# Kernel tuning notes

Hardware: AMD Instinct MI355X
Metric: run time of the kernel (lower is better)

The kernel has to match this reference:

```python
import jax, jax.numpy as jnp
from jax import lax
import numpy as np
import math

EMBED_DIM = 1024
NUM_HEADS = 16
REDUCTION = 2


def setup_inputs() -> dict:
    key = jax.random.key(0)
    ks = jax.random.split(key, 11)
    B, N, C = 2, 4096, EMBED_DIM
    s = 1.0 / math.sqrt(C)
    return {
        "x": jax.random.normal(ks[0], (B, N, C), jnp.float32),
        "q_w": jax.random.normal(ks[1], (C, C), jnp.float32) * s,
        "q_b": jax.random.normal(ks[2], (C,), jnp.float32) * s,
        "k_w": jax.random.normal(ks[3], (C, C), jnp.float32) * s,
        "k_b": jax.random.normal(ks[4], (C,), jnp.float32) * s,
        "v_w": jax.random.normal(ks[5], (C, C), jnp.float32) * s,
        "v_b": jax.random.normal(ks[6], (C,), jnp.float32) * s,
        "conv_w": jax.random.normal(ks[7], (C, 1, 3), jnp.float32) * 0.5,
        "conv_b": jax.random.normal(ks[8], (C,), jnp.float32) * 0.1,
        "out_w": jax.random.normal(ks[9], (C, C), jnp.float32) * s,
        "out_b": jax.random.normal(ks[10], (C,), jnp.float32) * s,
    }


def reference(x, q_w, q_b, k_w, k_b, v_w, v_b, conv_w, conv_b, out_w, out_b):
    B, N, C = x.shape
    H = NUM_HEADS
    D = C // H
    scale = 1.0 / math.sqrt(D)

    q = x @ q_w.T + q_b  # [B,N,C]

    # depthwise conv1d KV downsample: kernel=3, stride=REDUCTION, pad=1, groups=C
    xd = jnp.transpose(x, (0, 2, 1))  # [B,C,N]
    xd = lax.conv_general_dilated(
        xd, conv_w, window_strides=(REDUCTION,), padding=[(1, 1)],
        feature_group_count=C, dimension_numbers=("NCH", "OIH", "NCH"))
    xd = xd + conv_b[None, :, None]
    xd = jnp.transpose(xd, (0, 2, 1))  # [B,Nk,C]

    k = xd @ k_w.T + k_b
    v = xd @ v_w.T + v_b

    Nk = k.shape[1]
    q = q.reshape(B, N, H, D).transpose(0, 2, 1, 3)   # [B,H,N,D]
    k = k.reshape(B, Nk, H, D).transpose(0, 2, 1, 3)  # [B,H,Nk,D]
    v = v.reshape(B, Nk, H, D).transpose(0, 2, 1, 3)

    att = jnp.einsum("bhnd,bhmd->bhnm", q, k) * scale  # [B,H,N,Nk]
    att = jax.nn.softmax(att, axis=-1)
    out = jnp.einsum("bhnm,bhmd->bhnd", att, v)        # [B,H,N,D]
    out = out.transpose(0, 2, 1, 3).reshape(B, N, C)
    return out @ out_w.T + out_b
```

## Files before the change

### kernel.cpp

```cpp
#include <hip/hip_runtime.h>
#include <stdint.h>
#include <stddef.h>


using bf16x8 = __attribute__((ext_vector_type(8))) short;
using f32x4  = __attribute__((ext_vector_type(4))) float;
using f32x16 = __attribute__((ext_vector_type(16))) float;
using u16x4  = __attribute__((ext_vector_type(4))) unsigned short;
using u32x4  = __attribute__((ext_vector_type(4))) uint32_t;

#if defined(__has_builtin)
#if __has_builtin(__builtin_amdgcn_exp2f)
#define FAST_EXP2(x) __builtin_amdgcn_exp2f(x)
#endif
#endif
#ifndef FAST_EXP2
extern "C" __device__ float __ocml_native_exp2_f32(float);
#define FAST_EXP2(x) __ocml_native_exp2_f32(x)
#endif

__device__ __forceinline__ unsigned short f2bf(float f) {
  union { float f; uint32_t u; } v; v.f = f;
  uint32_t r = v.u + 0x7fffu + ((v.u >> 16) & 1u);
  return (unsigned short)(r >> 16);
}

__device__ __forceinline__ uint32_t cvt_pk_bf16(float lo, float hi) {
  uint32_t r;
  asm("v_cvt_pk_bf16_f32 %0, %1, %2" : "=v"(r) : "v"(lo), "v"(hi));
  return r;
}

__device__ __forceinline__ void plane32_swap(uint32_t& a, uint32_t& b) {
  asm("v_permlane32_swap_b32 %0, %1" : "+v"(a), "+v"(b));
}

__global__ __launch_bounds__(256)
void cast_bf16_kernel(const float* __restrict__ in, unsigned short* __restrict__ out, int n) {
  int i = (blockIdx.x * 256 + threadIdx.x) * 8;
  if (i >= n) return;
  float4 a = *(const float4*)(in + i);
  float4 b = *(const float4*)(in + i + 4);
  u16x4 r0 = {f2bf(a.x), f2bf(a.y), f2bf(a.z), f2bf(a.w)};
  u16x4 r1 = {f2bf(b.x), f2bf(b.y), f2bf(b.z), f2bf(b.w)};
  *(u16x4*)(out + i) = r0;
  *(u16x4*)(out + i + 4) = r1;
}

struct WPtrs { const float* p0; const float* p1; const float* p2; const float* p3; };
__global__ __launch_bounds__(256)
void cast4_bf16_kernel(WPtrs in, unsigned short* __restrict__ out) {
  int which = blockIdx.x >> 9;
  int i = ((blockIdx.x & 511) * 256 + threadIdx.x) * 8;
  const float* src = (which == 0) ? in.p0 : (which == 1) ? in.p1
                   : (which == 2) ? in.p2 : in.p3;
  unsigned short* dst = out + (size_t)which * 1048576;
  float4 a = *(const float4*)(src + i);
  float4 b = *(const float4*)(src + i + 4);
  u16x4 r0 = {f2bf(a.x), f2bf(a.y), f2bf(a.z), f2bf(a.w)};
  u16x4 r1 = {f2bf(b.x), f2bf(b.y), f2bf(b.z), f2bf(b.w)};
  *(u16x4*)(dst + i) = r0;
  *(u16x4*)(dst + i + 4) = r1;
}

__global__ __launch_bounds__(256)
void conv_ds_kernel(const float* __restrict__ x, const float* __restrict__ cw,
                    const float* __restrict__ cb, unsigned short* __restrict__ xd) {
  int row = blockIdx.x;
  int b = row >> 11, m = row & 2047;
  int c = threadIdx.x * 4;
  const float* xb = x + (size_t)b * 4096 * 1024;
  int n0 = 2 * m - 1;
  float4 x0 = {0.f, 0.f, 0.f, 0.f};
  if (n0 >= 0) x0 = *(const float4*)(xb + (size_t)n0 * 1024 + c);
  float4 x1 = *(const float4*)(xb + (size_t)(2 * m) * 1024 + c);
  float4 x2 = *(const float4*)(xb + (size_t)(2 * m + 1) * 1024 + c);
  float4 w0 = *(const float4*)(cw + c * 3);
  float4 w1 = *(const float4*)(cw + c * 3 + 4);
  float4 w2 = *(const float4*)(cw + c * 3 + 8);
  float4 bb = *(const float4*)(cb + c);
  float r0 = x0.x * w0.x + x1.x * w0.y + x2.x * w0.z + bb.x;
  float r1 = x0.y * w0.w + x1.y * w1.x + x2.y * w1.y + bb.y;
  float r2 = x0.z * w1.z + x1.z * w1.w + x2.z * w2.x + bb.z;
  float r3 = x0.w * w2.y + x1.w * w2.z + x2.w * w2.w + bb.w;
  u16x4 r = {f2bf(r0), f2bf(r1), f2bf(r2), f2bf(r3)};
  *(u16x4*)(xd + (size_t)row * 1024 + c) = r;
}

template<int OUT_MODE>
__global__ __launch_bounds__(256)
void gemm_bt(const unsigned short* __restrict__ A, const unsigned short* __restrict__ W,
             const float* __restrict__ bias, const float* __restrict__ bias2,
             void* __restrict__ out, void* __restrict__ out2,
             int M, int N, int K) {
  __shared__ unsigned short As[128 * 32];
  __shared__ unsigned short Bs[128 * 32];
  const int tid = threadIdx.x;
  const int w = tid >> 6, lane = tid & 63;
  const int nbn = N >> 7;
  const int bm = blockIdx.x / nbn, bn = blockIdx.x % nbn;
  const int wr = w >> 1, wc = w & 1;
  const int l15 = lane & 15, l4 = lane >> 4;

  f32x4 acc[4][4];
#pragma unroll
  for (int m = 0; m < 4; ++m)
#pragma unroll
    for (int n = 0; n < 4; ++n) acc[m][n] = (f32x4)0.0f;

  const int arow = bm * 128 + w * 16 + (lane >> 2);
  const int brow = bn * 128 + w * 16 + (lane >> 2);
  const int kcol = (lane & 3) * 8;

  for (int kt = 0; kt < K; kt += 32) {
#pragma unroll
    for (int p = 0; p < 2; ++p) {
      __builtin_amdgcn_global_load_lds(
          (const __attribute__((address_space(1))) void*)(A + (size_t)(arow + p * 64) * K + kt + kcol),
          (__attribute__((address_space(3))) void*)(As + p * 2048 + w * 512), 16, 0, 0);
      __builtin_amdgcn_global_load_lds(
          (const __attribute__((address_space(1))) void*)(W + (size_t)(brow + p * 64) * K + kt + kcol),
          (__attribute__((address_space(3))) void*)(Bs + p * 2048 + w * 512), 16, 0, 0);
    }
    __syncthreads();
    bf16x8 af[4], bf[4];
#pragma unroll
    for (int m = 0; m < 4; ++m) af[m] = *(const bf16x8*)(As + (wr * 64 + m * 16 + l15) * 32 + l4 * 8);
#pragma unroll
    for (int n = 0; n < 4; ++n) bf[n] = *(const bf16x8*)(Bs + (wc * 64 + n * 16 + l15) * 32 + l4 * 8);
#pragma unroll
    for (int m = 0; m < 4; ++m)
#pragma unroll
      for (int n = 0; n < 4; ++n)
        acc[m][n] = __builtin_amdgcn_mfma_f32_16x16x32_bf16(af[m], bf[n], acc[m][n], 0, 0, 0);
    __syncthreads();
  }

  const bool vregion = (OUT_MODE == 3) && (bn >= 8);
#pragma unroll
  for (int n = 0; n < 4; ++n) {
    int col = bn * 128 + wc * 64 + n * 16 + l15;
    float bv = vregion ? bias2[col - 1024] : bias[col];
#pragma unroll
    for (int m = 0; m < 4; ++m) {
      int row0 = bm * 128 + wr * 64 + m * 16 + l4 * 4;
      if (vregion) {
        int b = row0 >> 11, kv = row0 & 2047;
        u16x4 r = {f2bf(acc[m][n][0] + bv), f2bf(acc[m][n][1] + bv),
                   f2bf(acc[m][n][2] + bv), f2bf(acc[m][n][3] + bv)};
        *(u16x4*)((unsigned short*)out2 + ((size_t)(b * 1024 + (col - 1024))) * 2048 + kv) = r;
      } else if (OUT_MODE == 1 || OUT_MODE == 3) {
        const int ldn = (OUT_MODE == 3) ? 1024 : N;
#pragma unroll
        for (int i = 0; i < 4; ++i)
          ((unsigned short*)out)[(size_t)(row0 + i) * ldn + col] = f2bf(acc[m][n][i] + bv);
      } else {
#pragma unroll
        for (int i = 0; i < 4; ++i)
          ((float*)out)[(size_t)(row0 + i) * N + col] = acc[m][n][i] + bv;
      }
    }
  }
}

#define ATT_SCL_L2E 0.18033688011112043f

__global__ __launch_bounds__(256)
void flash_attn_kernel(const unsigned short* __restrict__ q,
                       const unsigned short* __restrict__ k,
                       const unsigned short* __restrict__ vt,
                       unsigned short* __restrict__ o) {
  const int bid = blockIdx.x;
  const int lin = (bid & 7) * 128 + (bid >> 3);
  const int qb = lin & 31;
  const int hb = lin >> 5;
  const int h = hb & 15, b = hb >> 4;

  const int tid = threadIdx.x;
  const int w = tid >> 6, lane = tid & 63;
  const int l31 = lane & 31, hi = lane >> 5;

  __shared__ unsigned short Ks[2][64 * 64];
  __shared__ unsigned short Vs[2][64 * 64];

  const size_t C = 1024;
  const int qrow = b * 4096 + qb * 128 + w * 32 + l31;

  bf16x8 qf[4];
#pragma unroll
  for (int ks = 0; ks < 4; ++ks)
    qf[ks] = *(const bf16x8*)(q + (size_t)qrow * C + h * 64 + ks * 16 + hi * 8);

  f32x16 o0 = (f32x16)0.0f, o1 = (f32x16)0.0f;
  float lrun = 0.f;

  const int srow = (tid & 7) | ((tid >> 5) << 3);
  const int sc2  = (tid >> 3) & 3;
  const int sxor = (srow & 7);
  const unsigned short* kbase = k  + ((size_t)(b * 2048 + srow)) * C + h * 64;
  const unsigned short* vbase = vt + ((size_t)(b * 1024 + h * 64 + srow)) * 2048;

  bf16x8 krg[2], vrg[2], tmp[2];
#pragma unroll
  for (int j = 0; j < 2; ++j) tmp[j] = *(const bf16x8*)(kbase + (sc2 + 4 * j) * 8);
#pragma unroll
  for (int j = 0; j < 2; ++j)
    *(bf16x8*)(&Ks[0][srow * 64 + (((sc2 + 4 * j) ^ sxor) * 8)]) = tmp[j];
#pragma unroll
  for (int j = 0; j < 2; ++j) tmp[j] = *(const bf16x8*)(kbase + (size_t)64 * C + (sc2 + 4 * j) * 8);
#pragma unroll
  for (int j = 0; j < 2; ++j)
    *(bf16x8*)(&Ks[1][srow * 64 + (((sc2 + 4 * j) ^ sxor) * 8)]) = tmp[j];
#pragma unroll
  for (int j = 0; j < 2; ++j) tmp[j] = *(const bf16x8*)(vbase + (sc2 + 4 * j) * 8);
#pragma unroll
  for (int j = 0; j < 2; ++j)
    *(bf16x8*)(&Vs[0][srow * 64 + (((sc2 + 4 * j) ^ sxor) * 8)]) = tmp[j];
#pragma unroll
  for (int j = 0; j < 2; ++j) {
    krg[j] = *(const bf16x8*)(kbase + (size_t)128 * C + (sc2 + 4 * j) * 8);
    vrg[j] = *(const bf16x8*)(vbase + 64 + (sc2 + 4 * j) * 8);
  }
  __syncthreads();

  const int r0 = l31, r1 = 32 + l31;
  const int x0c = (r0 & 7) * 8, x1c = (r1 & 7) * 8;

  f32x16 sA0 = (f32x16)0.0f, sA1 = (f32x16)0.0f;
  f32x16 sB0 = (f32x16)0.0f, sB1 = (f32x16)0.0f;
  __builtin_amdgcn_s_setprio(1);
#pragma unroll
  for (int ks = 0; ks < 4; ++ks) {
    int coff = ks * 16 + hi * 8;
    bf16x8 kf0 = *(const bf16x8*)(&Ks[0][r0 * 64 + (coff ^ x0c)]);
    bf16x8 kf1 = *(const bf16x8*)(&Ks[0][r1 * 64 + (coff ^ x1c)]);
    sA0 = __builtin_amdgcn_mfma_f32_32x32x16_bf16(kf0, qf[0 + ks - ks], sA0, 0, 0, 0);
    sA0 = sA0;
    sA0 = __builtin_amdgcn_mfma_f32_32x32x16_bf16(kf0, qf[ks], sA0, 0, 0, 0);
    sA1 = __builtin_amdgcn_mfma_f32_32x32x16_bf16(kf1, qf[ks], sA1, 0, 0, 0);
  }
  __builtin_amdgcn_s_setprio(0);
  sA0 = (f32x16)0.0f; sA1 = (f32x16)0.0f;
  __builtin_amdgcn_s_setprio(1);
#pragma unroll
  for (int ks = 0; ks < 4; ++ks) {
    int coff = ks * 16 + hi * 8;
    bf16x8 kf0 = *(const bf16x8*)(&Ks[0][r0 * 64 + (coff ^ x0c)]);
    bf16x8 kf1 = *(const bf16x8*)(&Ks[0][r1 * 64 + (coff ^ x1c)]);
    sA0 = __builtin_amdgcn_mfma_f32_32x32x16_bf16(kf0, qf[ks], sA0, 0, 0, 0);
    sA1 = __builtin_amdgcn_mfma_f32_32x32x16_bf16(kf1, qf[ks], sA1, 0, 0, 0);
  }
  __builtin_amdgcn_s_setprio(0);
  __syncthreads();

  auto body = [&](int t, f32x16& c0, f32x16& c1, f32x16& n0, f32x16& n1) {
    const unsigned short* Vc = Vs[t & 1];

    if (t < 31) {
      const unsigned short* Kn = Ks[(t + 1) & 1];
      n0 = (f32x16)0.0f; n1 = (f32x16)0.0f;
      __builtin_amdgcn_s_setprio(1);
#pragma unroll
      for (int ks = 0; ks < 4; ++ks) {
        int coff = ks * 16 + hi * 8;
        bf16x8 kf0 = *(const bf16x8*)(Kn + r0 * 64 + (coff ^ x0c));
        bf16x8 kf1 = *(const bf16x8*)(Kn + r1 * 64 + (coff ^ x1c));
        n0 = __builtin_amdgcn_mfma_f32_32x32x16_bf16(kf0, qf[ks], n0, 0, 0, 0);
        n1 = __builtin_amdgcn_mfma_f32_32x32x16_bf16(kf1, qf[ks], n1, 0, 0, 0);
      }
      __builtin_amdgcn_s_setprio(0);
    }

    float rs0 = 0.f, rs1 = 0.f;
#pragma unroll
    for (int i = 0; i < 16; ++i) {
      float p0 = FAST_EXP2(c0[i] * ATT_SCL_L2E);
      float p1 = FAST_EXP2(c1[i] * ATT_SCL_L2E);
      c0[i] = p0; c1[i] = p1;
      rs0 += p0; rs1 += p1;
    }
    lrun += rs0 + rs1;

    u32x4 pw[4];
#pragma unroll
    for (int hh = 0; hh < 2; ++hh) {
#pragma unroll
      for (int cp = 0; cp < 2; ++cp) {
#pragma unroll
        for (int e = 0; e < 2; ++e) {
          float xa0 = (hh == 0) ? c0[8 * cp + 2 * e]     : c1[8 * cp + 2 * e];
          float xa1 = (hh == 0) ? c0[8 * cp + 2 * e + 1] : c1[8 * cp + 2 * e + 1];
          float xb0 = (hh == 0) ? c0[8 * cp + 4 + 2 * e]     : c1[8 * cp + 4 + 2 * e];
          float xb1 = (hh == 0) ? c0[8 * cp + 4 + 2 * e + 1] : c1[8 * cp + 4 + 2 * e + 1];
          uint32_t wa = cvt_pk_bf16(xa0, xa1);
          uint32_t wb = cvt_pk_bf16(xb0, xb1);
          plane32_swap(wa, wb);
          pw[2 * hh + cp][e]     = wa;
          pw[2 * hh + cp][e + 2] = wb;
        }
      }
    }

    __builtin_amdgcn_s_setprio(1);
#pragma unroll
    for (int ksv = 0; ksv < 4; ++ksv) {
      bf16x8 pv = __builtin_bit_cast(bf16x8, pw[ksv]);
      int coff = ksv * 16 + hi * 8;
      bf16x8 vf0 = *(const bf16x8*)(Vc + r0 * 64 + (coff ^ x0c));
      bf16x8 vf1 = *(const bf16x8*)(Vc + r1 * 64 + (coff ^ x1c));
      o0 = __builtin_amdgcn_mfma_f32_32x32x16_bf16(vf0, pv, o0, 0, 0, 0);
      o1 = __builtin_amdgcn_mfma_f32_32x32x16_bf16(vf1, pv, o1, 0, 0, 0);
    }
    __builtin_amdgcn_s_setprio(0);

    if (t < 30) {
#pragma unroll
      for (int j = 0; j < 2; ++j)
        *(bf16x8*)(&((unsigned short*)Ks[t & 1])[srow * 64 + (((sc2 + 4 * j) ^ sxor) * 8)]) = krg[j];
    }
    if (t < 31) {
#pragma unroll
      for (int j = 0; j < 2; ++j)
        *(bf16x8*)(&((unsigned short*)Vs[(t + 1) & 1])[srow * 64 + (((sc2 + 4 * j) ^ sxor) * 8)]) = vrg[j];
    }
    if (t < 29) {
#pragma unroll
      for (int j = 0; j < 2; ++j)
        krg[j] = *(const bf16x8*)(kbase + (size_t)(t + 3) * 64 * C + (sc2 + 4 * j) * 8);
    }
    if (t < 30) {
#pragma unroll
      for (int j = 0; j < 2; ++j)
        vrg[j] = *(const bf16x8*)(vbase + (t + 2) * 64 + (sc2 + 4 * j) * 8);
    }
    if (t < 31) __syncthreads();
  };

  for (int tt = 0; tt < 16; ++tt) {
    body(2 * tt,     sA0, sA1, sB0, sB1);
    body(2 * tt + 1, sB0, sB1, sA0, sA1);
  }

  float lsum = lrun + __shfl_xor(lrun, 32);
  const float inv = 1.0f / lsum;
  u32x4 ow[4];
#pragma unroll
  for (int c = 0; c < 4; ++c) {
#pragma unroll
    for (int e = 0; e < 2; ++e) {
      uint32_t wa = cvt_pk_bf16(o0[4 * c + 2 * e] * inv, o0[4 * c + 2 * e + 1] * inv);
      uint32_t wb = cvt_pk_bf16(o1[4 * c + 2 * e] * inv, o1[4 * c + 2 * e + 1] * inv);
      plane32_swap(wa, wb);
      ow[c][e]     = wa;
      ow[c][e + 2] = wb;
    }
  }
  unsigned short* op = o + (size_t)qrow * C + h * 64 + hi * 32;
#pragma unroll
  for (int ch = 0; ch < 4; ++ch)
    *(u32x4*)(op + ch * 8) = ow[ch];
}

extern "C" void kernel_launch(void* const* d_in, const int* in_sizes, int n_in,
                              void* d_out, int out_size, void* d_ws, size_t ws_size,
                              hipStream_t stream) {
  const float* x   = (const float*)d_in[0];
  const float* q_w = (const float*)d_in[1];
  const float* q_b = (const float*)d_in[2];
  const float* k_w = (const float*)d_in[3];
  const float* k_b = (const float*)d_in[4];
  const float* v_w = (const float*)d_in[5];
  const float* v_b = (const float*)d_in[6];
  const float* cw  = (const float*)d_in[7];
  const float* cb  = (const float*)d_in[8];
  const float* o_w = (const float*)d_in[9];
  const float* o_b = (const float*)d_in[10];
  float* out = (float*)d_out;

  unsigned short* ws    = (unsigned short*)d_ws;
  unsigned short* x_bf  = ws;
  unsigned short* qw_bf = x_bf + 8388608;
  unsigned short* kw_bf = qw_bf + 1048576;
  unsigned short* vw_bf = kw_bf + 1048576;
  unsigned short* ow_bf = vw_bf + 1048576;
  unsigned short* q_bf  = ow_bf + 1048576;
  unsigned short* xd_bf = q_bf + 8388608;
  unsigned short* k_bf  = xd_bf + 4194304;
  unsigned short* vt_bf = k_bf + 4194304;
  unsigned short* ao_bf = x_bf;

  cast_bf16_kernel<<<4096, 256, 0, stream>>>(x, x_bf, 8388608);
  WPtrs wp = {q_w, k_w, v_w, o_w};
  cast4_bf16_kernel<<<2048, 256, 0, stream>>>(wp, qw_bf);
  conv_ds_kernel<<<4096, 256, 0, stream>>>(x, cw, cb, xd_bf);

  gemm_bt<1><<<512, 256, 0, stream>>>(x_bf, qw_bf, q_b, nullptr, q_bf, nullptr,
                                      8192, 1024, 1024);
  gemm_bt<3><<<512, 256, 0, stream>>>(xd_bf, kw_bf, k_b, v_b, k_bf, vt_bf,
                                      4096, 2048, 1024);

  flash_attn_kernel<<<1024, 256, 0, stream>>>(q_bf, k_bf, vt_bf, ao_bf);

  gemm_bt<0><<<512, 256, 0, stream>>>(ao_bf, ow_bf, o_b, nullptr, out, nullptr,
                                      8192, 1024, 1024);
}
```

Before: 209.7 us.

## Software-pipeline attention loop: carry packed probabilities and overlap exp with MFMAs

Restructures the attention inner loop so the next tile's QK scores are computed and then exp'd and packed into bf16 registers at the end of the current iteration. The loop now carries packed P words instead of fp32 score accumulators, so QK and PV MFMAs are issued back to back while the exp/pack work runs after the global loads. It also drops the duplicated warm-up QK computation in the prologue. The aim is better overlap of transcendental and VALU work with matrix instructions and fewer live fp32 registers, with some risk of scheduling changes or register pressure shifting.

```diff
diff --git a/kernel.cpp b/kernel.cpp
--- a/kernel.cpp
+++ b/kernel.cpp
@@ -200,98 +200,29 @@
   const unsigned short* kbase = k  + ((size_t)(b * 2048 + srow)) * C + h * 64;
   const unsigned short* vbase = vt + ((size_t)(b * 1024 + h * 64 + srow)) * 2048;
 
-  bf16x8 krg[2], vrg[2], tmp[2];
-#pragma unroll
-  for (int j = 0; j < 2; ++j) tmp[j] = *(const bf16x8*)(kbase + (sc2 + 4 * j) * 8);
-#pragma unroll
-  for (int j = 0; j < 2; ++j)
-    *(bf16x8*)(&Ks[0][srow * 64 + (((sc2 + 4 * j) ^ sxor) * 8)]) = tmp[j];
-#pragma unroll
-  for (int j = 0; j < 2; ++j) tmp[j] = *(const bf16x8*)(kbase + (size_t)64 * C + (sc2 + 4 * j) * 8);
-#pragma unroll
-  for (int j = 0; j < 2; ++j)
-    *(bf16x8*)(&Ks[1][srow * 64 + (((sc2 + 4 * j) ^ sxor) * 8)]) = tmp[j];
-#pragma unroll
-  for (int j = 0; j < 2; ++j) tmp[j] = *(const bf16x8*)(vbase + (sc2 + 4 * j) * 8);
-#pragma unroll
-  for (int j = 0; j < 2; ++j)
-    *(bf16x8*)(&Vs[0][srow * 64 + (((sc2 + 4 * j) ^ sxor) * 8)]) = tmp[j];
-#pragma unroll
-  for (int j = 0; j < 2; ++j) {
-    krg[j] = *(const bf16x8*)(kbase + (size_t)128 * C + (sc2 + 4 * j) * 8);
-    vrg[j] = *(const bf16x8*)(vbase + 64 + (sc2 + 4 * j) * 8);
-  }
-  __syncthreads();
-
   const int r0 = l31, r1 = 32 + l31;
   const int x0c = (r0 & 7) * 8, x1c = (r1 & 7) * 8;
 
-  f32x16 sA0 = (f32x16)0.0f, sA1 = (f32x16)0.0f;
-  f32x16 sB0 = (f32x16)0.0f, sB1 = (f32x16)0.0f;
-  __builtin_amdgcn_s_setprio(1);
-#pragma unroll
-  for (int ks = 0; ks < 4; ++ks) {
-    int coff = ks * 16 + hi * 8;
-    bf16x8 kf0 = *(const bf16x8*)(&Ks[0][r0 * 64 + (coff ^ x0c)]);
-    bf16x8 kf1 = *(const bf16x8*)(&Ks[0][r1 * 64 + (coff ^ x1c)]);
-    sA0 = __builtin_amdgcn_mfma_f32_32x32x16_bf16(kf0, qf[0 + ks - ks], sA0, 0, 0, 0);
-    sA0 = sA0;
-    sA0 = __builtin_amdgcn_mfma_f32_32x32x16_bf16(kf0, qf[ks], sA0, 0, 0, 0);
-    sA1 = __builtin_amdgcn_mfma_f32_32x32x16_bf16(kf1, qf[ks], sA1, 0, 0, 0);
-  }
-  __builtin_amdgcn_s_setprio(0);
-  sA0 = (f32x16)0.0f; sA1 = (f32x16)0.0f;
-  __builtin_amdgcn_s_setprio(1);
-#pragma unroll
-  for (int ks = 0; ks < 4; ++ks) {
-    int coff = ks * 16 + hi * 8;
-    bf16x8 kf0 = *(const bf16x8*)(&Ks[0][r0 * 64 + (coff ^ x0c)]);
-    bf16x8 kf1 = *(const bf16x8*)(&Ks[0][r1 * 64 + (coff ^ x1c)]);
-    sA0 = __builtin_amdgcn_mfma_f32_32x32x16_bf16(kf0, qf[ks], sA0, 0, 0, 0);
-    sA1 = __builtin_amdgcn_mfma_f32_32x32x16_bf16(kf1, qf[ks], sA1, 0, 0, 0);
-  }
-  __builtin_amdgcn_s_setprio(0);
-  __syncthreads();
-
-  auto body = [&](int t, f32x16& c0, f32x16& c1, f32x16& n0, f32x16& n1) {
-    const unsigned short* Vc = Vs[t & 1];
-
-    if (t < 31) {
-      const unsigned short* Kn = Ks[(t + 1) & 1];
-      n0 = (f32x16)0.0f; n1 = (f32x16)0.0f;
-      __builtin_amdgcn_s_setprio(1);
-#pragma unroll
-      for (int ks = 0; ks < 4; ++ks) {
-        int coff = ks * 16 + hi * 8;
-        bf16x8 kf0 = *(const bf16x8*)(Kn + r0 * 64 + (coff ^ x0c));
-        bf16x8 kf1 = *(const bf16x8*)(Kn + r1 * 64 + (coff ^ x1c));
-        n0 = __builtin_amdgcn_mfma_f32_32x32x16_bf16(kf0, qf[ks], n0, 0, 0, 0);
-        n1 = __builtin_amdgcn_mfma_f32_32x32x16_bf16(kf1, qf[ks], n1, 0, 0, 0);
-      }
-      __builtin_amdgcn_s_setprio(0);
-    }
-
+  auto exppack = [&](f32x16& s0, f32x16& s1, u32x4 (&pw)[4]) {
     float rs0 = 0.f, rs1 = 0.f;
 #pragma unroll
     for (int i = 0; i < 16; ++i) {
-      float p0 = FAST_EXP2(c0[i] * ATT_SCL_L2E);
-      float p1 = FAST_EXP2(c1[i] * ATT_SCL_L2E);
-      c0[i] = p0; c1[i] = p1;
+      float p0 = FAST_EXP2(s0[i] * ATT_SCL_L2E);
+      float p1 = FAST_EXP2(s1[i] * ATT_SCL_L2E);
+      s0[i] = p0; s1[i] = p1;
       rs0 += p0; rs1 += p1;
     }
     lrun += rs0 + rs1;
-
-    u32x4 pw[4];
 #pragma unroll
     for (int hh = 0; hh < 2; ++hh) {
 #pragma unroll
       for (int cp = 0; cp < 2; ++cp) {
 #pragma unroll
         for (int e = 0; e < 2; ++e) {
-          float xa0 = (hh == 0) ? c0[8 * cp + 2 * e]     : c1[8 * cp + 2 * e];
-          float xa1 = (hh == 0) ? c0[8 * cp + 2 * e + 1] : c1[8 * cp + 2 * e + 1];
-          float xb0 = (hh == 0) ? c0[8 * cp + 4 + 2 * e]     : c1[8 * cp + 4 + 2 * e];
-          float xb1 = (hh == 0) ? c0[8 * cp + 4 + 2 * e + 1] : c1[8 * cp + 4 + 2 * e + 1];
+          float xa0 = (hh == 0) ? s0[8 * cp + 2 * e]     : s1[8 * cp + 2 * e];
+          float xa1 = (hh == 0) ? s0[8 * cp + 2 * e + 1] : s1[8 * cp + 2 * e + 1];
+          float xb0 = (hh == 0) ? s0[8 * cp + 4 + 2 * e]     : s1[8 * cp + 4 + 2 * e];
+          float xb1 = (hh == 0) ? s0[8 * cp + 4 + 2 * e + 1] : s1[8 * cp + 4 + 2 * e + 1];
           uint32_t wa = cvt_pk_bf16(xa0, xa1);
           uint32_t wb = cvt_pk_bf16(xb0, xb1);
           plane32_swap(wa, wb);
@@ -300,11 +231,67 @@
         }
       }
     }
-
+  };
+
+  bf16x8 krg[2], vrg[2], tmp[2];
+#pragma unroll
+  for (int j = 0; j < 2; ++j) tmp[j] = *(const bf16x8*)(kbase + (sc2 + 4 * j) * 8);
+#pragma unroll
+  for (int j = 0; j < 2; ++j)
+    *(bf16x8*)(&Ks[0][srow * 64 + (((sc2 + 4 * j) ^ sxor) * 8)]) = tmp[j];
+#pragma unroll
+  for (int j = 0; j < 2; ++j) tmp[j] = *(const bf16x8*)(kbase + (size_t)64 * C + (sc2 + 4 * j) * 8);
+#pragma unroll
+  for (int j = 0; j < 2; ++j)
+    *(bf16x8*)(&Ks[1][srow * 64 + (((sc2 + 4 * j) ^ sxor) * 8)]) = tmp[j];
+#pragma unroll
+  for (int j = 0; j < 2; ++j) tmp[j] = *(const bf16x8*)(vbase + (sc2 + 4 * j) * 8);
+#pragma unroll
+  for (int j = 0; j < 2; ++j)
+    *(bf16x8*)(&Vs[0][srow * 64 + (((sc2 + 4 * j) ^ sxor) * 8)]) = tmp[j];
+#pragma unroll
+  for (int j = 0; j < 2; ++j) {
+    krg[j] = *(const bf16x8*)(kbase + (size_t)128 * C + (sc2 + 4 * j) * 8);
+    vrg[j] = *(const bf16x8*)(vbase + 64 + (sc2 + 4 * j) * 8);
+  }
+  __syncthreads();
+
+  u32x4 pwA[4], pwB[4];
+  {
+    f32x16 s0 = (f32x16)0.0f, s1 = (f32x16)0.0f;
     __builtin_amdgcn_s_setprio(1);
 #pragma unroll
+    for (int ks = 0; ks < 4; ++ks) {
+      int coff = ks * 16 + hi * 8;
+      bf16x8 kf0 = *(const bf16x8*)(&Ks[0][r0 * 64 + (coff ^ x0c)]);
+      bf16x8 kf1 = *(const bf16x8*)(&Ks[0][r1 * 64 + (coff ^ x1c)]);
+      s0 = __builtin_amdgcn_mfma_f32_32x32x16_bf16(kf0, qf[ks], s0, 0, 0, 0);
+      s1 = __builtin_amdgcn_mfma_f32_32x32x16_bf16(kf1, qf[ks], s1, 0, 0, 0);
+    }
+    __builtin_amdgcn_s_setprio(0);
+    exppack(s0, s1, pwA);
+  }
+  __syncthreads();
+
+  auto body = [&](int t, u32x4 (&pwC)[4], u32x4 (&pwN)[4]) {
+    const unsigned short* Vc = Vs[t & 1];
+    f32x16 s0 = (f32x16)0.0f, s1 = (f32x16)0.0f;
+
+    __builtin_amdgcn_s_setprio(1);
+    if (t < 31) {
+      const unsigned short* Kn = Ks[(t + 1) & 1];
+#pragma unroll
+      for (int ks = 0; ks < 4; ++ks) {
+        int coff = ks * 16 + hi * 8;
+        bf16x8 kf0 = *(const bf16x8*)(Kn + r0 * 64 + (coff ^ x0c));
+        bf16x8 kf1 = *(const bf16x8*)(Kn + r1 * 64 + (coff ^ x1c));
+        s0 = __builtin_amdgcn_mfma_f32_32x32x16_bf16(kf0, qf[ks], s0, 0, 0, 0);
+        s1 = __builtin_amdgcn_mfma_f32_32x32x16_bf16(kf1, qf[ks], s1, 0, 0, 0);
+      }
+    }
+#pragma unroll
     for (int ksv = 0; ksv < 4; ++ksv) {
-      bf16x8 pv = __builtin_bit_cast(bf16x8, pw[ksv]);
+      bf16x8 pv = __builtin_bit_cast(bf16x8, pwC[ksv]);
       int coff = ksv * 16 + hi * 8;
       bf16x8 vf0 = *(const bf16x8*)(Vc + r0 * 64 + (coff ^ x0c));
       bf16x8 vf1 = *(const bf16x8*)(Vc + r1 * 64 + (coff ^ x1c));
@@ -333,12 +320,15 @@
       for (int j = 0; j < 2; ++j)
         vrg[j] = *(const bf16x8*)(vbase + (t + 2) * 64 + (sc2 + 4 * j) * 8);
     }
+
+    if (t < 31) exppack(s0, s1, pwN);
+
     if (t < 31) __syncthreads();
   };
 
   for (int tt = 0; tt < 16; ++tt) {
-    body(2 * tt,     sA0, sA1, sB0, sB1);
-    body(2 * tt + 1, sB0, sB1, sA0, sA1);
+    body(2 * tt,     pwA, pwB);
+    body(2 * tt + 1, pwB, pwA);
   }
 
   float lsum = lrun + __shfl_xor(lrun, 32);
```

New measurement: 208.3 us. About the same (-0.7%).
